# Optimization experiments

Measured on AMD Instinct MI355X. Metric: run time of the kernel, lower is better.

The kernel has to match this reference:

```python
import jax, jax.numpy as jnp
import numpy as np


def _rope_tables(T, d):
    half = d // 2
    i = jnp.arange(half, dtype=jnp.float32)
    theta = 10000.0 ** (-2.0 * i / d)          # [half]
    m = jnp.arange(T, dtype=jnp.float32)[:, None]  # [T,1]
    ang = m * theta[None, :]                    # [T,half]
    return jnp.cos(ang), jnp.sin(ang)


def _rotate(v, cos, sin):
    # interleaved even/odd RoPE rotation, vectorized
    B, T, d = v.shape
    half = d // 2
    v2 = v.reshape(B, T, half, 2)
    even, odd = v2[..., 0], v2[..., 1]
    c = cos[None, :, :]
    s = sin[None, :, :]
    new_even = even * c - odd * s
    new_odd = even * s + odd * c
    return jnp.stack([new_even, new_odd], axis=-1).reshape(B, T, d)


def setup_inputs() -> dict:
    key = jax.random.key(0)
    k1, k2, k3, k4 = jax.random.split(key, 4)
    B, T, d = 4, 2048, 1024
    x = jax.random.normal(k1, (B, T, d), dtype=jnp.float32)
    scale = 0.02
    Wq = jax.random.normal(k2, (d, d), dtype=jnp.float32) * scale
    Wk = jax.random.normal(k3, (d, d), dtype=jnp.float32) * scale
    Wv = jax.random.normal(k4, (d, d), dtype=jnp.float32) * scale
    return {"x": x, "Wq": Wq, "Wk": Wk, "Wv": Wv}


def reference(x, Wq, Wk, Wv):
    B, T, d = x.shape
    cos, sin = _rope_tables(T, d)
    # torch Linear: y = x @ W.T
    Q = jnp.einsum('btd,ed->bte', x, Wq)
    K = jnp.einsum('btd,ed->bte', x, Wk)
    V = jnp.einsum('btd,ed->bte', x, Wv)
    Qr = _rotate(Q, cos, sin)
    Kr = _rotate(K, cos, sin)
    scores = jnp.einsum('bqd,bkd->bqk', Qr, Kr) / jnp.sqrt(jnp.float32(d))
    # NOTE: original uses tril with diagonal=1 (allows one future position)
    mask = jnp.tril(jnp.ones((T, T), dtype=bool), k=1)
    scores = jnp.where(mask[None, :, :], scores, -jnp.inf)
    attn = jax.nn.softmax(scores, axis=-1)
    out = jnp.einsum('bqk,bkd->bqd', attn, V)
    return out
```

## Files before the change

kernel.cpp:

```cpp
#include <hip/hip_runtime.h>


typedef float f32x4 __attribute__((ext_vector_type(4)));
typedef __bf16 bf16x8 __attribute__((ext_vector_type(8)));

#define BM 128
#define BN 128
#define BK 64

__device__ __forceinline__ unsigned short f2bf(float f) {
  union { float f; unsigned int u; } c; c.f = f;
  unsigned int u = c.u;
  u += 0x7fffu + ((u >> 16) & 1u);
  return (unsigned short)(u >> 16);
}
__device__ __forceinline__ float bf2f(unsigned short h) {
  union { unsigned int u; float f; } c; c.u = ((unsigned int)h) << 16;
  return c.f;
}

__device__ __forceinline__ void async16(const unsigned short* gp, unsigned short* lp) {
  __builtin_amdgcn_global_load_lds(
      (const __attribute__((address_space(1))) void*)gp,
      (__attribute__((address_space(3))) void*)lp, 16, 0, 0);
}

__global__ __launch_bounds__(256) void cvt_all(
    const float4* __restrict__ x, const float4* __restrict__ wq,
    const float4* __restrict__ wk, const float4* __restrict__ wv,
    ushort4* __restrict__ xb, ushort4* __restrict__ wb,
    float4* __restrict__ rowsums) {
  int b = blockIdx.x, t = threadIdx.x;
  if (b == 11264) {
#pragma unroll
    for (int i = 0; i < 8; ++i) rowsums[i * 256 + t] = float4{0.f, 0.f, 0.f, 0.f};
    return;
  }
  const float4* src;
  ushort4* dst;
  long i;
  if (b < 8192) { src = x; dst = xb; i = (long)b * 256 + t; }
  else if (b < 9216) { src = wq; dst = wb; i = (long)(b - 8192) * 256 + t; }
  else if (b < 10240) { src = wk; dst = wb + 262144; i = (long)(b - 9216) * 256 + t; }
  else { src = wv; dst = wb + 524288; i = (long)(b - 10240) * 256 + t; }
  float4 v = src[i];
  ushort4 o;
  o.x = f2bf(v.x); o.y = f2bf(v.y); o.z = f2bf(v.z); o.w = f2bf(v.w);
  dst[i] = o;
}

template <int IM, int JN>
__device__ __forceinline__ void gemm_body(
    const unsigned short* __restrict__ A, const unsigned short* __restrict__ B,
    unsigned short* As, unsigned short* Bs,
    int lda, int ldb, int m0, int n0, int ktiles,
    int tid, int lane, int wave, f32x4 (&acc)[IM][JN]) {
  const int wm = (wave >> 1) * (IM * 16);
  const int wn = (wave & 1) * (JN * 16);
  const int fm = lane & 15;
  const int q = lane >> 4;
  const int srow = tid >> 3;
  const int c = (tid & 7) ^ (srow & 7);
  const unsigned short* Ab = A + (long)(m0 + srow) * lda + c * 8;
  const unsigned short* Bb = B + (long)(n0 + srow) * ldb + c * 8;
  unsigned short* ldA = As + tid * 8;
  unsigned short* ldB = Bs + tid * 8;

  for (int kt = 0; kt < ktiles; ++kt) {
    const long k0 = (long)kt * BK;
    __syncthreads();
#pragma unroll
    for (int p = 0; p < IM; ++p)
      async16(Ab + (long)(p * 32) * lda + k0, ldA + p * 2048);
#pragma unroll
    for (int p = 0; p < JN; ++p)
      async16(Bb + (long)(p * 32) * ldb + k0, ldB + p * 2048);
    __syncthreads();

#pragma unroll
    for (int s = 0; s < 2; ++s) {
      bf16x8 af[IM], bfr[JN];
#pragma unroll
      for (int i = 0; i < IM; ++i) {
        int row = wm + i * 16 + fm;
        af[i] = *(const bf16x8*)&As[row * 64 + ((((s << 2) | q) ^ (row & 7)) << 3)];
      }
#pragma unroll
      for (int j = 0; j < JN; ++j) {
        int row = wn + j * 16 + fm;
        bfr[j] = *(const bf16x8*)&Bs[row * 64 + ((((s << 2) | q) ^ (row & 7)) << 3)];
      }
#pragma unroll
      for (int i = 0; i < IM; ++i)
#pragma unroll
        for (int j = 0; j < JN; ++j)
          acc[i][j] = __builtin_amdgcn_mfma_f32_16x16x32_bf16(af[i], bfr[j], acc[i][j], 0, 0, 0);
    }
  }
}

__global__ __launch_bounds__(256, 3) void qkv_rope_gemm(
    const unsigned short* __restrict__ A, const unsigned short* __restrict__ B,
    unsigned short* __restrict__ Qr, unsigned short* __restrict__ Kr,
    unsigned short* __restrict__ Vt) {
  __shared__ __align__(16) unsigned short As[BM * BK];
  __shared__ __align__(16) unsigned short Bs[BN * BK];
  const int tid = threadIdx.x, lane = tid & 63, wave = tid >> 6;
  const int bm = blockIdx.x, bn = blockIdx.y;
  const int m0 = bm * BM, n0 = bn * BN;
  const int wm = (wave >> 1) * 64, wn = (wave & 1) * 64;
  const int q = lane >> 4, fm = lane & 15;

  f32x4 acc[4][4];
#pragma unroll
  for (int i = 0; i < 4; ++i)
#pragma unroll
    for (int j = 0; j < 4; ++j) acc[i][j] = (f32x4)(0.f);

  gemm_body<4, 4>(A, B, As, Bs, 1024, 1024, m0, n0, 16, tid, lane, wave, acc);

  if (n0 < 2048) {
    const float NEG = -13.287712379549449f / 1024.f;
    unsigned short* dst = (n0 < 1024) ? Qr : Kr;
    const int t00 = (m0 + wm + q * 4) & 2047;
#pragma unroll
    for (int j = 0; j < 4; ++j) {
      int c = (n0 & 1023) + wn + j * 16 + fm;
      float th = exp2f((float)(c & ~1) * NEG);
      float sgn = (c & 1) ? 1.f : -1.f;
      float ang0 = (float)t00 * th;
      float cb = __cosf(ang0), sb = __sinf(ang0);
      float c1 = __cosf(th), s1 = __sinf(th);
      float c16 = __cosf(16.f * th), s16 = __sinf(16.f * th);
#pragma unroll
      for (int i = 0; i < 4; ++i) {
        int gmB = m0 + wm + i * 16 + q * 4;
        float cr = cb, sr = sb;
#pragma unroll
        for (int r = 0; r < 4; ++r) {
          float v = acc[i][j][r];
          float p = __shfl_xor(v, 1);
          dst[(long)(gmB + r) * 1024 + c] = f2bf(v * cr + sgn * p * sr);
          float crn = cr * c1 - sr * s1;
          sr = sr * c1 + cr * s1;
          cr = crn;
        }
        float cbn = cb * c16 - sb * s16;
        sb = sb * c16 + cb * s16;
        cb = cbn;
      }
    }
  } else {
    const int c0 = n0 - 2048;
#pragma unroll
    for (int j = 0; j < 4; ++j) {
      int c = c0 + wn + j * 16 + fm;
#pragma unroll
      for (int i = 0; i < 4; ++i) {
        int gmB = m0 + wm + i * 16 + q * 4;
        int b = gmB >> 11, t = gmB & 2047;
        ushort4 pk;
        pk.x = f2bf(acc[i][j][0]);
        pk.y = f2bf(acc[i][j][1]);
        pk.z = f2bf(acc[i][j][2]);
        pk.w = f2bf(acc[i][j][3]);
        *(ushort4*)&Vt[((long)b * 1024 + c) * 2048 + t] = pk;
      }
    }
  }
}

__global__ __launch_bounds__(256, 3) void s_gemm(
    const unsigned short* __restrict__ Qr, const unsigned short* __restrict__ Kr,
    unsigned short* __restrict__ Sb, float* __restrict__ rowsums) {
  __shared__ __align__(16) unsigned short As[BM * BK];
  __shared__ __align__(16) unsigned short Bs[BN * BK];
  const int tid = threadIdx.x, lane = tid & 63, wave = tid >> 6;
  const int z = blockIdx.z;
  int idx = blockIdx.x, bm = 0;
#pragma unroll 1
  for (; bm < 16; ++bm) {
    int cnt = (bm + 2 > 16) ? 16 : bm + 2;
    if (idx < cnt) break;
    idx -= cnt;
  }
  const int bn = idx;
  const unsigned short* A = Qr + (long)z * 2048 * 1024;
  const unsigned short* B = Kr + (long)z * 2048 * 1024;
  unsigned short* S = Sb + (long)z * 2048 * 2048;
  float* rs = rowsums + (long)z * 2048;
  const int m0 = bm * BM, n0 = bn * BN;
  const int wm = (wave >> 1) * 64, wn = (wave & 1) * 64;
  const int q = lane >> 4, fm = lane & 15;

  f32x4 acc[4][4];
#pragma unroll
  for (int i = 0; i < 4; ++i)
#pragma unroll
    for (int j = 0; j < 4; ++j) acc[i][j] = (f32x4)(0.f);

  gemm_body<4, 4>(A, B, As, Bs, 1024, 1024, m0, n0, 16, tid, lane, wave, acc);

  float* rsum = (float*)Bs;
  __syncthreads();
  if (tid < 128) rsum[tid] = 0.f;
  __syncthreads();

#pragma unroll
  for (int i = 0; i < 4; ++i) {
    int gmB = m0 + wm + i * 16 + q * 4;
    float ps[4] = {0.f, 0.f, 0.f, 0.f};
#pragma unroll
    for (int j = 0; j < 4; ++j) {
      int gn = n0 + wn + j * 16 + fm;
#pragma unroll
      for (int r = 0; r < 4; ++r) {
        float e = (gn <= gmB + r + 1) ? __expf(acc[i][j][r] * 0.03125f) : 0.f;
        unsigned short h = f2bf(e);
        S[(long)(gmB + r) * 2048 + gn] = h;
        ps[r] += bf2f(h);
      }
    }
#pragma unroll
    for (int r = 0; r < 4; ++r) {
      float v = ps[r];
      v += __shfl_xor(v, 1);
      v += __shfl_xor(v, 2);
      v += __shfl_xor(v, 4);
      v += __shfl_xor(v, 8);
      if (fm == 0) atomicAdd(&rsum[wm + i * 16 + q * 4 + r], v);
    }
  }
  __syncthreads();
  if (tid < 128) atomicAdd(&rs[m0 + tid], rsum[tid]);
}

__global__ __launch_bounds__(256, 3) void pv_gemm(
    const unsigned short* __restrict__ Sb, const unsigned short* __restrict__ Vt,
    const float* __restrict__ rowsums, float* __restrict__ out, int b0) {
  __shared__ __align__(16) unsigned short As[64 * BK];
  __shared__ __align__(16) unsigned short Bs[128 * BK];
  const int tid = threadIdx.x, lane = tid & 63, wave = tid >> 6;
  const int bn = blockIdx.x & 7;
  const int z = blockIdx.x >> 3;
  const int bm = 31 - blockIdx.y;
  const unsigned short* A = Sb + (long)z * 2048 * 2048;
  const unsigned short* B = Vt + (long)(b0 + z) * 1024 * 2048;
  const float* rs = rowsums + (long)(b0 + z) * 2048;
  float* C = out + (long)(b0 + z) * 2048 * 1024;
  int ktiles = bm + 2;
  if (ktiles > 32) ktiles = 32;
  const int m0 = bm * 64, n0 = bn * 128;
  const int wm = (wave >> 1) * 32, wn = (wave & 1) * 64;
  const int q = lane >> 4, fm = lane & 15;

  f32x4 acc[2][4];
#pragma unroll
  for (int i = 0; i < 2; ++i)
#pragma unroll
    for (int j = 0; j < 4; ++j) acc[i][j] = (f32x4)(0.f);

  gemm_body<2, 4>(A, B, As, Bs, 2048, 2048, m0, n0, ktiles, tid, lane, wave, acc);

#pragma unroll
  for (int i = 0; i < 2; ++i) {
    int gmB = m0 + wm + i * 16 + q * 4;
#pragma unroll
    for (int r = 0; r < 4; ++r) {
      float inv = 1.f / rs[gmB + r];
#pragma unroll
      for (int j = 0; j < 4; ++j) {
        int gn = n0 + wn + j * 16 + fm;
        C[(long)(gmB + r) * 1024 + gn] = acc[i][j][r] * inv;
      }
    }
  }
}

extern "C" void kernel_launch(void* const* d_in, const int* in_sizes, int n_in,
                              void* d_out, int out_size, void* d_ws, size_t ws_size,
                              hipStream_t stream) {
  const float* x = (const float*)d_in[0];
  const float* Wq = (const float*)d_in[1];
  const float* Wk = (const float*)d_in[2];
  const float* Wv = (const float*)d_in[3];
  float* out = (float*)d_out;

  float* rowsums = (float*)d_ws;
  unsigned short* Qr = (unsigned short*)d_ws + 16384;
  unsigned short* Kr = Qr + (long)8192 * 1024;
  unsigned short* Vt = Kr + (long)8192 * 1024;
  unsigned short* xb = Vt + (long)8192 * 1024;
  unsigned short* Wb = xb + (long)8192 * 1024;
  unsigned short* Sb = xb;

  int BCH = 4;
  while (BCH > 1 && (size_t)32768 + (size_t)(48 + 8 * BCH) * 1024 * 1024 > ws_size)
    BCH >>= 1;

  cvt_all<<<11265, 256, 0, stream>>>((const float4*)x, (const float4*)Wq,
                                     (const float4*)Wk, (const float4*)Wv,
                                     (ushort4*)xb, (ushort4*)Wb, (float4*)rowsums);

  qkv_rope_gemm<<<dim3(64, 24), 256, 0, stream>>>(xb, Wb, Qr, Kr, Vt);

  for (int b0 = 0; b0 < 4; b0 += BCH) {
    s_gemm<<<dim3(151, 1, BCH), 256, 0, stream>>>(Qr + (long)b0 * 2048 * 1024,
                                                  Kr + (long)b0 * 2048 * 1024,
                                                  Sb, rowsums + (long)b0 * 2048);
    pv_gemm<<<dim3(8 * BCH, 32), 256, 0, stream>>>(Sb, Vt, rowsums, out, b0);
  }
}
```

Measured before the change: 218.9 us.

## Pack causal score blocks into compact per-row-band storage, launch all batches at once

```diff
diff --git a/kernel.cpp b/kernel.cpp
--- a/kernel.cpp
+++ b/kernel.cpp
@@ -7,6 +7,8 @@
 #define BM 128
 #define BN 128
 #define BK 64
+
+#define SP_BATCH 2473984
 
 __device__ __forceinline__ unsigned short f2bf(float f) {
   union { float f; unsigned int u; } c; c.f = f;
@@ -172,7 +174,7 @@
 
 __global__ __launch_bounds__(256, 3) void s_gemm(
     const unsigned short* __restrict__ Qr, const unsigned short* __restrict__ Kr,
-    unsigned short* __restrict__ Sb, float* __restrict__ rowsums) {
+    unsigned short* __restrict__ Sp, float* __restrict__ rowsums) {
   __shared__ __align__(16) unsigned short As[BM * BK];
   __shared__ __align__(16) unsigned short Bs[BN * BK];
   const int tid = threadIdx.x, lane = tid & 63, wave = tid >> 6;
@@ -187,7 +189,8 @@
   const int bn = idx;
   const unsigned short* A = Qr + (long)z * 2048 * 1024;
   const unsigned short* B = Kr + (long)z * 2048 * 1024;
-  unsigned short* S = Sb + (long)z * 2048 * 2048;
+  const int len = ((bm + 2 > 16) ? 16 : bm + 2) * 128;
+  unsigned short* S = Sp + (long)z * SP_BATCH + (long)(bm * (bm + 3) / 2) * 16384;
   float* rs = rowsums + (long)z * 2048;
   const int m0 = bm * BM, n0 = bn * BN;
   const int wm = (wave >> 1) * 64, wn = (wave & 1) * 64;
@@ -209,6 +212,7 @@
 #pragma unroll
   for (int i = 0; i < 4; ++i) {
     int gmB = m0 + wm + i * 16 + q * 4;
+    int lrow = wm + i * 16 + q * 4;
     float ps[4] = {0.f, 0.f, 0.f, 0.f};
 #pragma unroll
     for (int j = 0; j < 4; ++j) {
@@ -217,7 +221,7 @@
       for (int r = 0; r < 4; ++r) {
         float e = (gn <= gmB + r + 1) ? __expf(acc[i][j][r] * 0.03125f) : 0.f;
         unsigned short h = f2bf(e);
-        S[(long)(gmB + r) * 2048 + gn] = h;
+        S[(long)(lrow + r) * len + gn] = h;
         ps[r] += bf2f(h);
       }
     }
@@ -236,18 +240,22 @@
 }
 
 __global__ __launch_bounds__(256, 3) void pv_gemm(
-    const unsigned short* __restrict__ Sb, const unsigned short* __restrict__ Vt,
-    const float* __restrict__ rowsums, float* __restrict__ out, int b0) {
+    const unsigned short* __restrict__ Sp, const unsigned short* __restrict__ Vt,
+    const float* __restrict__ rowsums, float* __restrict__ out) {
   __shared__ __align__(16) unsigned short As[64 * BK];
   __shared__ __align__(16) unsigned short Bs[128 * BK];
   const int tid = threadIdx.x, lane = tid & 63, wave = tid >> 6;
   const int bn = blockIdx.x & 7;
   const int z = blockIdx.x >> 3;
   const int bm = 31 - blockIdx.y;
-  const unsigned short* A = Sb + (long)z * 2048 * 2048;
-  const unsigned short* B = Vt + (long)(b0 + z) * 1024 * 2048;
-  const float* rs = rowsums + (long)(b0 + z) * 2048;
-  float* C = out + (long)(b0 + z) * 2048 * 1024;
+  const int sb = bm >> 1;
+  const int lda = ((sb + 2 > 16) ? 16 : sb + 2) * 128;
+  const unsigned short* A = Sp + (long)z * SP_BATCH +
+                            (long)(sb * (sb + 3) / 2) * 16384 +
+                            (long)(bm & 1) * 64 * lda;
+  const unsigned short* B = Vt + (long)z * 1024 * 2048;
+  const float* rs = rowsums + (long)z * 2048;
+  float* C = out + (long)z * 2048 * 1024;
   int ktiles = bm + 2;
   if (ktiles > 32) ktiles = 32;
   const int m0 = bm * 64, n0 = bn * 128;
@@ -260,7 +268,7 @@
 #pragma unroll
     for (int j = 0; j < 4; ++j) acc[i][j] = (f32x4)(0.f);
 
-  gemm_body<2, 4>(A, B, As, Bs, 2048, 2048, m0, n0, ktiles, tid, lane, wave, acc);
+  gemm_body<2, 4>(A, B, As, Bs, lda, 2048, 0, n0, ktiles, tid, lane, wave, acc);
 
 #pragma unroll
   for (int i = 0; i < 2; ++i) {
@@ -292,11 +300,6 @@
   unsigned short* Vt = Kr + (long)8192 * 1024;
   unsigned short* xb = Vt + (long)8192 * 1024;
   unsigned short* Wb = xb + (long)8192 * 1024;
-  unsigned short* Sb = xb;
-
-  int BCH = 4;
-  while (BCH > 1 && (size_t)32768 + (size_t)(48 + 8 * BCH) * 1024 * 1024 > ws_size)
-    BCH >>= 1;
 
   cvt_all<<<11265, 256, 0, stream>>>((const float4*)x, (const float4*)Wq,
                                      (const float4*)Wk, (const float4*)Wv,
@@ -304,10 +307,7 @@
 
   qkv_rope_gemm<<<dim3(64, 24), 256, 0, stream>>>(xb, Wb, Qr, Kr, Vt);
 
-  for (int b0 = 0; b0 < 4; b0 += BCH) {
-    s_gemm<<<dim3(151, 1, BCH), 256, 0, stream>>>(Qr + (long)b0 * 2048 * 1024,
-                                                  Kr + (long)b0 * 2048 * 1024,
-                                                  Sb, rowsums + (long)b0 * 2048);
-    pv_gemm<<<dim3(8 * BCH, 32), 256, 0, stream>>>(Sb, Vt, rowsums, out, b0);
-  }
-}
+  unsigned short* Sp = xb;
+  s_gemm<<<dim3(151, 1, 4), 256, 0, stream>>>(Qr, Kr, Sp, rowsums);
+  pv_gemm<<<dim3(32, 32), 256, 0, stream>>>(Sp, Vt, rowsums, out);
+}
```

Result: no change. 222.3 us (+1.6%).
